# Performance work log

Hardware: AMD Instinct MI355X
Metric: run time of the kernel (lower is better)

Reference implementation:

```python
import jax, jax.numpy as jnp
import numpy as np

BINS = 6
THRESH = 0.2
OUT_HW = (240, 240)


def _normalize(x, lo=0.0, hi=1.0):
    # torch: if max-min==0 return zeros, else affine rescale to [lo, hi]
    mn, mx = x.min(), x.max()
    rng = mx - mn
    safe = jnp.where(rng == 0, 1.0, rng)
    out = (x - mn) / safe * (hi - lo) + lo
    return jnp.where(rng == 0, jnp.zeros_like(x), out)


def _ponder(x):
    w = (x.max() - x.mean()) ** 2
    return _normalize(x) * w


def _zero_border(x):
    # zero first/last row and column (works batched over leading dims)
    return (x.at[..., 0, :].set(0.0)
             .at[..., :, 0].set(0.0)
             .at[..., -1, :].set(0.0)
             .at[..., :, -1].set(0.0))


def _rarity(ch):
    # ch: [H, W] single feature channel
    ch = _zero_border(ch)
    ch = _normalize(ch, 0.0, 256.0)
    # torch.histc(bins=BINS, min=0, max=256): last bin includes the max value
    bin_idx = jnp.clip(jnp.floor(ch / (256.0 / BINS)), 0, BINS - 1).astype(jnp.int32)
    hist = jnp.zeros((BINS,), ch.dtype).at[bin_idx].add(1.0)
    hist = -jnp.log(hist / hist.sum() + 0.0001)
    # (channel * bins - 1).long().clamp(0, bins-1): .long() truncates toward zero
    gidx = jnp.clip(jnp.trunc(ch * BINS - 1.0), 0, BINS - 1).astype(jnp.int32)
    dst = _normalize(hist[gidx], 0.0, 1.0)
    return _ponder(dst)


def _apply_rarity(layer):
    # layer: [1, C, H, W] -> per-channel rarity, ponderated sum, threshold
    ch = layer[0]  # [C, H, W]
    r = jax.vmap(_rarity)(ch)  # [C, H, W]
    rz = _zero_border(r)
    # channel 0 keeps its border (torch code only zeroes borders for i >= 1)
    maps = jnp.concatenate([r[:1], rz[1:]], axis=0)
    proc = jax.vmap(_ponder)(maps).sum(0)
    proc = _normalize(proc, 0.0, 1.0)
    return jnp.where(proc < THRESH, 0.0, proc)


def _group(layer):
    resized = jax.image.resize(_apply_rarity(layer), OUT_HW, 'bilinear')
    # pack of one layer: fuse_itti == map_ponderation of the single map
    return _normalize(_ponder(resized), 0.0, 256.0)


def _forward(l1, l2, l3, l4, l5):
    groups = jnp.stack([_group(l) for l in (l1, l2, l3, l4, l5)], axis=-1)  # [240,240,5]
    return groups.sum(-1), groups


def setup_inputs() -> dict:
    key = jax.random.key(0)
    ks = jax.random.split(key, 5)
    shapes = [(1, 64, 480, 480), (1, 128, 240, 240), (1, 256, 120, 120),
              (1, 512, 60, 60), (1, 512, 30, 30)]
    return {f"l{i+1}": jax.random.uniform(ks[i], shapes[i], jnp.float32)
            for i in range(5)}


def reference(l1, l2, l3, l4, l5):
    return _forward(l1, l2, l3, l4, l5)
```

## Files before the change

kernel.cpp:

```cpp
#include <hip/hip_runtime.h>
#include <math.h>

#define TPB 256

constexpr int DIMS_[5]  = {480, 240, 120, 60, 30};
constexpr int CHS_ [5]  = {64, 128, 256, 512, 512};
constexpr int CHB_ [5]  = {0, 64, 192, 448, 960};
constexpr int TOTCH     = 1472;
constexpr int PROCB_[5] = {0, 230400, 288000, 302400, 306000};
constexpr int PROCTOT   = 306900;

constexpr int O_CHMIN = 0;
constexpr int O_CHMAX = 1472;
constexpr int O_HIST  = 2944;
constexpr int O_GCNT  = 11776;
constexpr int O_CLUT  = 20608;
constexpr int O_BSUM  = O_CLUT + 16 * 1472;
constexpr int O_PMIN  = O_BSUM + 5;
constexpr int O_PMAX  = O_PMIN + 5;
constexpr int O_S3MIN = O_PMAX + 5;
constexpr int O_S3MAX = O_S3MIN + 5;
constexpr int O_S3SUM = O_S3MAX + 5;
constexpr int O_PROC  = 44192;
constexpr int O_RESZ  = O_PROC + PROCTOT;
constexpr int N_INIT  = O_PROC + PROCTOT;

struct P {
  const float* in[5];
  float* ws;
};

__device__ __forceinline__ void mk_hthr(float mn, float rng, float* th) {
  if (rng == 0.0f) { th[0]=th[1]=th[2]=th[3]=th[4]=INFINITY; return; }
  th[0] = mn + rng * (1.0f / 6.0f); th[1] = mn + rng * (2.0f / 6.0f);
  th[2] = mn + rng * (3.0f / 6.0f); th[3] = mn + rng * (4.0f / 6.0f);
  th[4] = mn + rng * (5.0f / 6.0f);
}
__device__ __forceinline__ void mk_gthr(float mn, float rng, float* tg) {
  if (rng == 0.0f) { tg[0]=tg[1]=tg[2]=tg[3]=tg[4]=INFINITY; return; }
  tg[0] = mn + rng * (2.0f / 1536.0f); tg[1] = mn + rng * (3.0f / 1536.0f);
  tg[2] = mn + rng * (4.0f / 1536.0f); tg[3] = mn + rng * (5.0f / 1536.0f);
  tg[4] = mn + rng * (6.0f / 1536.0f);
}

__global__ void k_init(float* ws) {
  int i = blockIdx.x * TPB + threadIdx.x;
  if (i >= N_INIT) return;
  unsigned v = 0u;
  if (i < O_CHMAX) v = 0x7F800000u;
  else if (i >= O_PMIN  && i < O_PMAX)  v = 0x7F800000u;
  else if (i >= O_S3MIN && i < O_S3MAX) v = 0x7F800000u;
  ((unsigned*)ws)[i] = v;
}

template <int L>
__device__ void bodyA(int local, const float* __restrict__ in, float* ws) {
  constexpr int D = DIMS_[L], HW = D * D, HW4 = HW / 4;
  constexpr int BPC = (HW4 + 4095) / 4096;
  int ch = local / BPC, chunk = local % BPC;
  int nvec = HW4 - chunk * 4096; if (nvec > 4096) nvec = 4096;
  const float4* pv = (const float4*)(in + (size_t)ch * HW) + (size_t)chunk * 4096;
  int t = threadIdx.x;
  float mn = INFINITY, mx = 0.0f;
  for (int i = 0; i < 16; i++) {
    int vi = i * TPB + t;
    if (vi < nvec) {
      float4 v = pv[vi];
      float vv[4] = {v.x, v.y, v.z, v.w};
      int e0 = (chunk * 4096 + vi) * 4;
      #pragma unroll
      for (int j = 0; j < 4; j++) {
        int e = e0 + j, y = e / D, x = e - y * D;
        bool inr = ((unsigned)(x - 1) < (unsigned)(D - 2)) && ((unsigned)(y - 1) < (unsigned)(D - 2));
        float s = inr ? vv[j] : 0.0f;
        mn = fminf(mn, s); mx = fmaxf(mx, s);
      }
    }
  }
  for (int o = 32; o; o >>= 1) { mn = fminf(mn, __shfl_down(mn, o)); mx = fmaxf(mx, __shfl_down(mx, o)); }
  __shared__ float smn[4], smx[4];
  int w = t >> 6;
  if ((t & 63) == 0) { smn[w] = mn; smx[w] = mx; }
  __syncthreads();
  if (t == 0) {
    mn = fminf(fminf(smn[0], smn[1]), fminf(smn[2], smn[3]));
    mx = fmaxf(fmaxf(smx[0], smx[1]), fmaxf(smx[2], smx[3]));
    int g = CHB_[L] + ch;
    atomicMin((unsigned*)ws + O_CHMIN + g, __float_as_uint(mn));
    atomicMax((unsigned*)ws + O_CHMAX + g, __float_as_uint(mx));
  }
}
__global__ void kA(P p) {
  int b = blockIdx.x;
  if      (b <  960) bodyA<0>(b,        p.in[0], p.ws);
  else if (b < 1472) bodyA<1>(b -  960, p.in[1], p.ws);
  else if (b < 1728) bodyA<2>(b - 1472, p.in[2], p.ws);
  else if (b < 2240) bodyA<3>(b - 1728, p.in[3], p.ws);
  else               bodyA<4>(b - 2240, p.in[4], p.ws);
}

template <int L>
__device__ void bodyB(int local, const float* __restrict__ in, float* ws) {
  constexpr int D = DIMS_[L], HW = D * D, HW4 = HW / 4;
  constexpr int BPC = (HW4 + 4095) / 4096;
  constexpr int DQ = D / 4;
  int ch = local / BPC, chunk = local % BPC;
  int g = CHB_[L] + ch;
  float mn = ws[O_CHMIN + g], mx = ws[O_CHMAX + g], rng = mx - mn;
  float th[5], tg[5];
  mk_hthr(mn, rng, th);
  mk_gthr(mn, rng, tg);
  int nvec = HW4 - chunk * 4096; if (nvec > 4096) nvec = 4096;
  const float4* pv = (const float4*)(in + (size_t)ch * HW) + (size_t)chunk * 4096;
  int t = threadIdx.x;
  unsigned cH0 = 0, cH1 = 0, cH2 = 0, cH3 = 0, cH4 = 0;
  unsigned cG0 = 0, cG1 = 0, cG2 = 0, cG3 = 0, cG4 = 0, nv4 = 0;
  for (int i = 0; i < 16; i++) {
    int vi = i * TPB + t;
    if (vi < nvec) {
      float4 v = pv[vi];
      float vv[4] = {v.x, v.y, v.z, v.w};
      int f4i = chunk * 4096 + vi;
      if constexpr (D % 4 == 0) {
        int y = f4i / DQ, xq = f4i - y * DQ;
        if (y == 0 || y == D - 1) { vv[0] = vv[1] = vv[2] = vv[3] = 0.0f; }
        else {
          if (xq == 0)      vv[0] = 0.0f;
          if (xq == DQ - 1) vv[3] = 0.0f;
        }
      } else {
        int e0 = f4i * 4;
        #pragma unroll
        for (int j = 0; j < 4; j++) {
          int e = e0 + j, y = e / D, x = e - y * D;
          bool inr = ((unsigned)(x - 1) < (unsigned)(D - 2)) && ((unsigned)(y - 1) < (unsigned)(D - 2));
          if (!inr) vv[j] = 0.0f;
        }
      }
      nv4 += __popcll(__ballot(1));
      #pragma unroll
      for (int j = 0; j < 4; j++) {
        float x = vv[j];
        cH0 += __popcll(__ballot(x >= th[0])); cH1 += __popcll(__ballot(x >= th[1]));
        cH2 += __popcll(__ballot(x >= th[2])); cH3 += __popcll(__ballot(x >= th[3]));
        cH4 += __popcll(__ballot(x >= th[4]));
        cG0 += __popcll(__ballot(x >= tg[0])); cG1 += __popcll(__ballot(x >= tg[1]));
        cG2 += __popcll(__ballot(x >= tg[2])); cG3 += __popcll(__ballot(x >= tg[3]));
        cG4 += __popcll(__ballot(x >= tg[4]));
      }
    }
  }
  if ((t & 63) == 0) {
    unsigned tot = nv4 * 4u;
    unsigned* H = (unsigned*)ws + O_HIST + g * 6;
    unsigned* G = (unsigned*)ws + O_GCNT + g * 6;
    atomicAdd(H + 0, tot - cH0); atomicAdd(H + 1, cH0 - cH1);
    atomicAdd(H + 2, cH1 - cH2); atomicAdd(H + 3, cH2 - cH3);
    atomicAdd(H + 4, cH3 - cH4); atomicAdd(H + 5, cH4);
    atomicAdd(G + 0, tot - cG0); atomicAdd(G + 1, cG0 - cG1);
    atomicAdd(G + 2, cG1 - cG2); atomicAdd(G + 3, cG2 - cG3);
    atomicAdd(G + 4, cG3 - cG4); atomicAdd(G + 5, cG4);
  }
}
__global__ void kB(P p) {
  int b = blockIdx.x;
  if      (b <  960) bodyB<0>(b,        p.in[0], p.ws);
  else if (b < 1472) bodyB<1>(b -  960, p.in[1], p.ws);
  else if (b < 1728) bodyB<2>(b - 1472, p.in[2], p.ws);
  else if (b < 2240) bodyB<3>(b - 1728, p.in[3], p.ws);
  else               bodyB<4>(b - 2240, p.in[4], p.ws);
}

__global__ void kS(P p) {
  int ch = blockIdx.x * TPB + threadIdx.x;
  if (ch >= TOTCH) return;
  float* ws = p.ws;
  int l = (ch < 64) ? 0 : (ch < 192) ? 1 : (ch < 448) ? 2 : (ch < 960) ? 3 : 4;
  int D = DIMS_[l];
  int HW = D * D;
  int c0 = ch - CHB_[l];
  unsigned hc[6], gc[6];
  unsigned* H = (unsigned*)ws + O_HIST + ch * 6;
  unsigned* G = (unsigned*)ws + O_GCNT + ch * 6;
  #pragma unroll
  for (int k = 0; k < 6; k++) { hc[k] = H[k]; gc[k] = G[k]; }
  float HWf = (float)HW;
  float nh[6];
  #pragma unroll
  for (int k = 0; k < 6; k++) nh[k] = -logf((float)hc[k] / HWf + 1e-4f);
  float dmn = INFINITY, dmx = -INFINITY;
  #pragma unroll
  for (int k = 0; k < 6; k++) if (gc[k]) { dmn = fminf(dmn, nh[k]); dmx = fmaxf(dmx, nh[k]); }
  float dr = dmx - dmn;
  float dstn[6];
  #pragma unroll
  for (int k = 0; k < 6; k++) dstn[k] = (dr == 0.0f) ? 0.0f : ((nh[k] - dmn) / dr);
  float maxv = (dr == 0.0f) ? 0.0f : 1.0f;
  double s1 = 0.0;
  #pragma unroll
  for (int k = 0; k < 6; k++) s1 += (double)gc[k] * (double)dstn[k];
  float mean1 = (float)(s1 / (double)HW);
  float w1 = maxv - mean1; w1 *= w1;
  float lut1[6];
  #pragma unroll
  for (int k = 0; k < 6; k++) lut1[k] = dstn[k] * w1;
  float mnc = ws[O_CHMIN + ch], mxc = ws[O_CHMAX + ch];
  float tg[5];
  mk_gthr(mnc, mxc - mnc, tg);
  int gb = (0.0f >= tg[0]) + (0.0f >= tg[1]) + (0.0f >= tg[2]) + (0.0f >= tg[3]) + (0.0f >= tg[4]);
  unsigned bcnt = (unsigned)(4 * D - 4);
  float lmn, lmx;
  double s2 = 0.0;
  if (c0 == 0) {
    lmn = INFINITY; lmx = -INFINITY;
    #pragma unroll
    for (int k = 0; k < 6; k++) if (gc[k]) {
      lmn = fminf(lmn, lut1[k]); lmx = fmaxf(lmx, lut1[k]);
      s2 += (double)gc[k] * (double)lut1[k];
    }
  } else {
    lmn = 0.0f; lmx = 0.0f;
    #pragma unroll
    for (int k = 0; k < 6; k++) {
      unsigned ic = gc[k] - ((k == gb) ? bcnt : 0u);
      if (ic) {
        lmn = fminf(lmn, lut1[k]); lmx = fmaxf(lmx, lut1[k]);
        s2 += (double)ic * (double)lut1[k];
      }
    }
  }
  float mean2 = (float)(s2 / (double)HW);
  float w2 = lmx - mean2; w2 *= w2;
  float r2 = lmx - lmn;
  float lout[6];
  #pragma unroll
  for (int k = 0; k < 6; k++) lout[k] = (r2 == 0.0f) ? 0.0f : (((lut1[k] - lmn) / r2) * w2);
  float* T = ws + O_CLUT + (size_t)ch * 16;
  #pragma unroll
  for (int k = 0; k < 5; k++) T[5 + k] = tg[k];
  #pragma unroll
  for (int k = 0; k < 6; k++) T[10 + k] = lout[k];
  float bc = (c0 == 0) ? lout[gb] : ((r2 == 0.0f) ? 0.0f : (((0.0f - lmn) / r2) * w2));
  atomicAdd(ws + O_BSUM + l, bc);
}

template <int L>
__device__ void bodyC(int local, const float* __restrict__ in, float* ws,
                      float* slut, float* sred) {
  constexpr int D = DIMS_[L], HW = D * D, HW4 = HW / 4, C = CHS_[L];
  constexpr int NT  = (HW4 + 63) / 64;
  constexpr int NCH = C / 64;
  int tile = local % NT, chunk = local / NT;
  int cbase = CHB_[L] + chunk * 64;
  int t = threadIdx.x, lane = t & 63, w = t >> 6;
  const float* gl = ws + O_CLUT + (size_t)cbase * 16;
  for (int i = t; i < 1024; i += TPB) slut[i] = gl[i];
  __syncthreads();
  int p4 = tile * 64 + lane;
  bool valid = p4 < HW4;
  float a0 = 0.0f, a1 = 0.0f, a2 = 0.0f, a3 = 0.0f;
  if (valid) {
    const float4* bp = (const float4*)in + (size_t)(chunk * 64 + w * 16) * HW4 + p4;
    const float* su = slut + (w * 16) * 16;
    #pragma unroll 4
    for (int c = 0; c < 16; c++) {
      float4 v = bp[(size_t)c * HW4];
      const float* cl = su + c * 16 + 5;
      float g0 = cl[0], g1 = cl[1], g2 = cl[2], g3 = cl[3], g4 = cl[4];
      float l0 = cl[5], l1 = cl[6], l2 = cl[7], l3 = cl[8], l4 = cl[9], l5 = cl[10];
      float s;
      s = (v.x >= g0) ? l1 : l0; s = (v.x >= g1) ? l2 : s; s = (v.x >= g2) ? l3 : s;
      s = (v.x >= g3) ? l4 : s;  s = (v.x >= g4) ? l5 : s; a0 += s;
      s = (v.y >= g0) ? l1 : l0; s = (v.y >= g1) ? l2 : s; s = (v.y >= g2) ? l3 : s;
      s = (v.y >= g3) ? l4 : s;  s = (v.y >= g4) ? l5 : s; a1 += s;
      s = (v.z >= g0) ? l1 : l0; s = (v.z >= g1) ? l2 : s; s = (v.z >= g2) ? l3 : s;
      s = (v.z >= g3) ? l4 : s;  s = (v.z >= g4) ? l5 : s; a2 += s;
      s = (v.w >= g0) ? l1 : l0; s = (v.w >= g1) ? l2 : s; s = (v.w >= g2) ? l3 : s;
      s = (v.w >= g3) ? l4 : s;  s = (v.w >= g4) ? l5 : s; a3 += s;
    }
  }
  sred[0 * 256 + w * 64 + lane] = a0;
  sred[1 * 256 + w * 64 + lane] = a1;
  sred[2 * 256 + w * 64 + lane] = a2;
  sred[3 * 256 + w * 64 + lane] = a3;
  __syncthreads();
  if (w == 0 && valid) {
    float o[4];
    #pragma unroll
    for (int j = 0; j < 4; j++)
      o[j] = sred[j * 256 + lane] + sred[j * 256 + 64 + lane] +
             sred[j * 256 + 128 + lane] + sred[j * 256 + 192 + lane];
    float bs = ws[O_BSUM + L];
    float* procL = ws + O_PROC + PROCB_[L];
    int px0 = p4 * 4;
    if constexpr (NCH == 1) {
      #pragma unroll
      for (int j = 0; j < 4; j++) {
        int px = px0 + j, y = px / D, x = px - y * D;
        bool inr = ((unsigned)(x - 1) < (unsigned)(D - 2)) && ((unsigned)(y - 1) < (unsigned)(D - 2));
        if (!inr) o[j] = bs;
      }
      ((float4*)procL)[p4] = make_float4(o[0], o[1], o[2], o[3]);
    } else {
      #pragma unroll
      for (int j = 0; j < 4; j++) {
        int px = px0 + j, y = px / D, x = px - y * D;
        bool inr = ((unsigned)(x - 1) < (unsigned)(D - 2)) && ((unsigned)(y - 1) < (unsigned)(D - 2));
        if (inr) atomicAdd(procL + px, o[j]);
        else if (chunk == 0) procL[px] = bs;
      }
    }
  }
}
__global__ __launch_bounds__(TPB) void kC(P p) {
  __shared__ float slut[1024];
  __shared__ float sred[1024];
  int b = blockIdx.x;
  if      (b <  900) bodyC<0>(b,        p.in[0], p.ws, slut, sred);
  else if (b < 1350) bodyC<1>(b -  900, p.in[1], p.ws, slut, sred);
  else if (b < 1578) bodyC<2>(b - 1350, p.in[2], p.ws, slut, sred);
  else if (b < 1698) bodyC<3>(b - 1578, p.in[3], p.ws, slut, sred);
  else               bodyC<4>(b - 1698, p.in[4], p.ws, slut, sred);
}

template <int L>
__device__ void bodyD(int chunk, float* ws) {
  constexpr int HW = DIMS_[L] * DIMS_[L];
  const float* pr = ws + O_PROC + PROCB_[L];
  int t = threadIdx.x;
  float mn = INFINITY, mx = 0.0f;
  #pragma unroll
  for (int i = 0; i < 16; i++) {
    int idx = chunk * 4096 + i * TPB + t;
    if (idx < HW) { float v = pr[idx]; mn = fminf(mn, v); mx = fmaxf(mx, v); }
  }
  for (int o = 32; o; o >>= 1) { mn = fminf(mn, __shfl_down(mn, o)); mx = fmaxf(mx, __shfl_down(mx, o)); }
  __shared__ float smn[4], smx[4];
  int w = t >> 6;
  if ((t & 63) == 0) { smn[w] = mn; smx[w] = mx; }
  __syncthreads();
  if (t == 0) {
    mn = fminf(fminf(smn[0], smn[1]), fminf(smn[2], smn[3]));
    mx = fmaxf(fmaxf(smx[0], smx[1]), fmaxf(smx[2], smx[3]));
    atomicMin((unsigned*)ws + O_PMIN + L, __float_as_uint(mn));
    atomicMax((unsigned*)ws + O_PMAX + L, __float_as_uint(mx));
  }
}
__global__ void kD(P p) {
  int b = blockIdx.x;
  if      (b < 57) bodyD<0>(b,      p.ws);
  else if (b < 72) bodyD<1>(b - 57, p.ws);
  else if (b < 76) bodyD<2>(b - 72, p.ws);
  else if (b < 77) bodyD<3>(b - 76, p.ws);
  else             bodyD<4>(b - 77, p.ws);
}

template <int L>
__device__ float bodyF(int px, float* ws) {
  constexpr int D = DIMS_[L];
  constexpr float INV = (float)D / 240.0f;
  constexpr float KS = (INV > 1.0f) ? INV : 1.0f;
  int oy = px / 240, ox = px - oy * 240;
  float mnv = __uint_as_float(((unsigned*)ws)[O_PMIN + L]);
  float mxv = __uint_as_float(((unsigned*)ws)[O_PMAX + L]);
  float pr = mxv - mnv;
  const float* procL = ws + O_PROC + PROCB_[L];
  float sfy = ((float)oy + 0.5f) * INV - 0.5f;
  float sfx = ((float)ox + 0.5f) * INV - 0.5f;
  int y0 = (int)ceilf(sfy - KS);  if (y0 < 0) y0 = 0;
  int y1 = (int)floorf(sfy + KS); if (y1 > D - 1) y1 = D - 1;
  int x0 = (int)ceilf(sfx - KS);  if (x0 < 0) x0 = 0;
  int x1 = (int)floorf(sfx + KS); if (x1 > D - 1) x1 = D - 1;
  float wsx = 0.0f;
  for (int jx = x0; jx <= x1; jx++) wsx += fmaxf(1.0f - fabsf(sfx - (float)jx) / KS, 0.0f);
  float acc = 0.0f, wsy = 0.0f;
  for (int jy = y0; jy <= y1; jy++) {
    float wy = fmaxf(1.0f - fabsf(sfy - (float)jy) / KS, 0.0f);
    wsy += wy;
    if (wy > 0.0f) {
      const float* row = procL + jy * D;
      float rs = 0.0f;
      for (int jx = x0; jx <= x1; jx++) {
        float wx = fmaxf(1.0f - fabsf(sfx - (float)jx) / KS, 0.0f);
        if (wx > 0.0f) {
          float v = row[jx];
          float tv = (pr == 0.0f) ? 0.0f : ((v - mnv) / pr);
          tv = (tv < 0.2f) ? 0.0f : tv;
          rs += wx * tv;
        }
      }
      acc += wy * rs;
    }
  }
  return acc / (wsy * wsx);
}
__global__ void kF(P p) {
  float* ws = p.ws;
  int b = blockIdx.x, l = b / 225;
  int px = (b - l * 225) * TPB + threadIdx.x;
  float res;
  switch (l) {
    case 0: res = bodyF<0>(px, ws); break;
    case 1: res = bodyF<1>(px, ws); break;
    case 2: res = bodyF<2>(px, ws); break;
    case 3: res = bodyF<3>(px, ws); break;
    default: res = bodyF<4>(px, ws); break;
  }
  ws[O_RESZ + l * 57600 + px] = res;
  float mn = res, mx = res, s = res;
  for (int o = 32; o; o >>= 1) {
    mn = fminf(mn, __shfl_down(mn, o));
    mx = fmaxf(mx, __shfl_down(mx, o));
    s += __shfl_down(s, o);
  }
  __shared__ float smn[4], smx[4], ssm[4];
  int t = threadIdx.x, w = t >> 6;
  if ((t & 63) == 0) { smn[w] = mn; smx[w] = mx; ssm[w] = s; }
  __syncthreads();
  if (t == 0) {
    mn = fminf(fminf(smn[0], smn[1]), fminf(smn[2], smn[3]));
    mx = fmaxf(fmaxf(smx[0], smx[1]), fmaxf(smx[2], smx[3]));
    s = ssm[0] + ssm[1] + ssm[2] + ssm[3];
    atomicMin((unsigned*)ws + O_S3MIN + l, __float_as_uint(mn));
    atomicMax((unsigned*)ws + O_S3MAX + l, __float_as_uint(mx));
    atomicAdd(ws + O_S3SUM + l, s);
  }
}

__global__ void kG2(P p, float* __restrict__ out) {
  float* ws = p.ws;
  int px = blockIdx.x * TPB + threadIdx.x;
  float sum = 0.0f;
  #pragma unroll
  for (int l = 0; l < 5; l++) {
    float v = ws[O_RESZ + l * 57600 + px];
    float mn3 = __uint_as_float(((unsigned*)ws)[O_S3MIN + l]);
    float mx3 = __uint_as_float(((unsigned*)ws)[O_S3MAX + l]);
    float mean3 = ws[O_S3SUM + l] / 57600.0f;
    float r3 = mx3 - mn3;
    float ov;
    if (r3 == 0.0f) ov = 0.0f;
    else {
      float w3 = mx3 - mean3; w3 *= w3;
      if (w3 == 0.0f) ov = 0.0f;
      else ov = ((v - mn3) / r3) * w3 / w3 * 256.0f;
    }
    out[57600 + px * 5 + l] = ov;
    sum += ov;
  }
  out[px] = sum;
}

extern "C" void kernel_launch(void* const* d_in, const int* in_sizes, int n_in,
                              void* d_out, int out_size, void* d_ws, size_t ws_size,
                              hipStream_t stream) {
  (void)in_sizes; (void)n_in; (void)out_size; (void)ws_size;
  P p;
  for (int i = 0; i < 5; i++) p.in[i] = (const float*)d_in[i];
  p.ws = (float*)d_ws;
  float* out = (float*)d_out;

  k_init<<<(N_INIT + TPB - 1) / TPB, TPB, 0, stream>>>(p.ws);
  kA  <<<2752, TPB, 0, stream>>>(p);
  kB  <<<2752, TPB, 0, stream>>>(p);
  kS  <<<6,    TPB, 0, stream>>>(p);
  kC  <<<1730, TPB, 0, stream>>>(p);
  kD  <<<78,   TPB, 0, stream>>>(p);
  kF  <<<1125, TPB, 0, stream>>>(p);
  kG2 <<<225,  TPB, 0, stream>>>(p, out);
}
```

Measured before the change: 294.0 us.

## Batch loads in stats passes, fuse layer-0 proc min/max into kC, shrink init

The min/max and histogram passes now issue four float4 loads up front before reducing, which raises memory-level parallelism. Border zeroing moves into a shared helper. For layer 0 (a single chunk per pixel), kC computes the proc min/max with wave shuffles and atomics as it writes, so kD no longer reads back the large 480x480 map. k_init now zeroes only the proc region that multi-chunk layers accumulate into. Out-of-range lanes in kB are filled with -inf so the ballot counts stay correct.

New measurement: 314.0 us. 6.8% more time.

```diff
diff --git a/kernel.cpp b/kernel.cpp
--- a/kernel.cpp
+++ b/kernel.cpp
@@ -23,7 +23,9 @@
 constexpr int O_S3SUM = O_S3MAX + 5;
 constexpr int O_PROC  = 44192;
 constexpr int O_RESZ  = O_PROC + PROCTOT;
-constexpr int N_INIT  = O_PROC + PROCTOT;
+constexpr int N_STAT  = O_PROC;
+constexpr int N_PZ    = PROCTOT - PROCB_[1];
+constexpr int N_INIT  = N_STAT + N_PZ;
 
 struct P {
   const float* in[5];
@@ -43,14 +45,40 @@
   tg[4] = mn + rng * (6.0f / 1536.0f);
 }
 
+template <int D>
+__device__ __forceinline__ void border_zero_f4(int f4i, float4& v) {
+  constexpr int DQ = D / 4;
+  if constexpr (D % 4 == 0) {
+    int y = f4i / DQ, xq = f4i - y * DQ;
+    if (y == 0 || y == D - 1) { v.x = v.y = v.z = v.w = 0.0f; }
+    else {
+      if (xq == 0)      v.x = 0.0f;
+      if (xq == DQ - 1) v.w = 0.0f;
+    }
+  } else {
+    int e0 = f4i * 4;
+    float* c = (float*)&v;
+    #pragma unroll
+    for (int j = 0; j < 4; j++) {
+      int e = e0 + j, y = e / D, x = e - y * D;
+      bool inr = ((unsigned)(x - 1) < (unsigned)(D - 2)) && ((unsigned)(y - 1) < (unsigned)(D - 2));
+      if (!inr) c[j] = 0.0f;
+    }
+  }
+}
+
 __global__ void k_init(float* ws) {
   int i = blockIdx.x * TPB + threadIdx.x;
   if (i >= N_INIT) return;
-  unsigned v = 0u;
-  if (i < O_CHMAX) v = 0x7F800000u;
-  else if (i >= O_PMIN  && i < O_PMAX)  v = 0x7F800000u;
-  else if (i >= O_S3MIN && i < O_S3MAX) v = 0x7F800000u;
-  ((unsigned*)ws)[i] = v;
+  if (i < N_STAT) {
+    unsigned v = 0u;
+    if (i < O_CHMAX) v = 0x7F800000u;
+    else if (i >= O_PMIN  && i < O_PMAX)  v = 0x7F800000u;
+    else if (i >= O_S3MIN && i < O_S3MAX) v = 0x7F800000u;
+    ((unsigned*)ws)[i] = v;
+  } else {
+    ws[O_PROC + PROCB_[1] + (i - N_STAT)] = 0.0f;
+  }
 }
 
 template <int L>
@@ -58,23 +86,27 @@
   constexpr int D = DIMS_[L], HW = D * D, HW4 = HW / 4;
   constexpr int BPC = (HW4 + 4095) / 4096;
   int ch = local / BPC, chunk = local % BPC;
-  int nvec = HW4 - chunk * 4096; if (nvec > 4096) nvec = 4096;
-  const float4* pv = (const float4*)(in + (size_t)ch * HW) + (size_t)chunk * 4096;
+  int base = chunk * 4096;
+  int nvec = HW4 - base; if (nvec > 4096) nvec = 4096;
+  const float4* pv = (const float4*)(in + (size_t)ch * HW) + base;
   int t = threadIdx.x;
   float mn = INFINITY, mx = 0.0f;
-  for (int i = 0; i < 16; i++) {
-    int vi = i * TPB + t;
-    if (vi < nvec) {
-      float4 v = pv[vi];
-      float vv[4] = {v.x, v.y, v.z, v.w};
-      int e0 = (chunk * 4096 + vi) * 4;
-      #pragma unroll
-      for (int j = 0; j < 4; j++) {
-        int e = e0 + j, y = e / D, x = e - y * D;
-        bool inr = ((unsigned)(x - 1) < (unsigned)(D - 2)) && ((unsigned)(y - 1) < (unsigned)(D - 2));
-        float s = inr ? vv[j] : 0.0f;
-        mn = fminf(mn, s); mx = fmaxf(mx, s);
-      }
+  for (int o = 0; o < 4; o++) {
+    float4 v[4];
+    #pragma unroll
+    for (int q = 0; q < 4; q++) {
+      int vi = (o * 4 + q) * TPB + t;
+      float4 vv = make_float4(0.0f, 0.0f, 0.0f, 0.0f);
+      if (vi < nvec) {
+        vv = pv[vi];
+        border_zero_f4<D>(base + vi, vv);
+      }
+      v[q] = vv;
+    }
+    #pragma unroll
+    for (int q = 0; q < 4; q++) {
+      mn = fminf(mn, fminf(fminf(v[q].x, v[q].y), fminf(v[q].z, v[q].w)));
+      mx = fmaxf(mx, fmaxf(fmaxf(v[q].x, v[q].y), fmaxf(v[q].z, v[q].w)));
     }
   }
   for (int o = 32; o; o >>= 1) { mn = fminf(mn, __shfl_down(mn, o)); mx = fmaxf(mx, __shfl_down(mx, o)); }
@@ -103,41 +135,35 @@
 __device__ void bodyB(int local, const float* __restrict__ in, float* ws) {
   constexpr int D = DIMS_[L], HW = D * D, HW4 = HW / 4;
   constexpr int BPC = (HW4 + 4095) / 4096;
-  constexpr int DQ = D / 4;
   int ch = local / BPC, chunk = local % BPC;
   int g = CHB_[L] + ch;
   float mn = ws[O_CHMIN + g], mx = ws[O_CHMAX + g], rng = mx - mn;
   float th[5], tg[5];
   mk_hthr(mn, rng, th);
   mk_gthr(mn, rng, tg);
-  int nvec = HW4 - chunk * 4096; if (nvec > 4096) nvec = 4096;
-  const float4* pv = (const float4*)(in + (size_t)ch * HW) + (size_t)chunk * 4096;
+  int base = chunk * 4096;
+  int nvec = HW4 - base; if (nvec > 4096) nvec = 4096;
+  const float4* pv = (const float4*)(in + (size_t)ch * HW) + base;
   int t = threadIdx.x;
   unsigned cH0 = 0, cH1 = 0, cH2 = 0, cH3 = 0, cH4 = 0;
   unsigned cG0 = 0, cG1 = 0, cG2 = 0, cG3 = 0, cG4 = 0, nv4 = 0;
-  for (int i = 0; i < 16; i++) {
-    int vi = i * TPB + t;
-    if (vi < nvec) {
-      float4 v = pv[vi];
-      float vv[4] = {v.x, v.y, v.z, v.w};
-      int f4i = chunk * 4096 + vi;
-      if constexpr (D % 4 == 0) {
-        int y = f4i / DQ, xq = f4i - y * DQ;
-        if (y == 0 || y == D - 1) { vv[0] = vv[1] = vv[2] = vv[3] = 0.0f; }
-        else {
-          if (xq == 0)      vv[0] = 0.0f;
-          if (xq == DQ - 1) vv[3] = 0.0f;
-        }
-      } else {
-        int e0 = f4i * 4;
-        #pragma unroll
-        for (int j = 0; j < 4; j++) {
-          int e = e0 + j, y = e / D, x = e - y * D;
-          bool inr = ((unsigned)(x - 1) < (unsigned)(D - 2)) && ((unsigned)(y - 1) < (unsigned)(D - 2));
-          if (!inr) vv[j] = 0.0f;
-        }
-      }
-      nv4 += __popcll(__ballot(1));
+  for (int o = 0; o < 4; o++) {
+    float4 v[4];
+    #pragma unroll
+    for (int q = 0; q < 4; q++) {
+      int vi = (o * 4 + q) * TPB + t;
+      float4 vv = make_float4(-INFINITY, -INFINITY, -INFINITY, -INFINITY);
+      if (vi < nvec) {
+        vv = pv[vi];
+        border_zero_f4<D>(base + vi, vv);
+      }
+      v[q] = vv;
+    }
+    #pragma unroll
+    for (int q = 0; q < 4; q++) {
+      int vi = (o * 4 + q) * TPB + t;
+      nv4 += __popcll(__ballot(vi < nvec));
+      float vv[4] = {v[q].x, v[q].y, v[q].z, v[q].w};
       #pragma unroll
       for (int j = 0; j < 4; j++) {
         float x = vv[j];
@@ -284,7 +310,7 @@
   sred[2 * 256 + w * 64 + lane] = a2;
   sred[3 * 256 + w * 64 + lane] = a3;
   __syncthreads();
-  if (w == 0 && valid) {
+  if (w == 0) {
     float o[4];
     #pragma unroll
     for (int j = 0; j < 4; j++)
@@ -294,14 +320,24 @@
     float* procL = ws + O_PROC + PROCB_[L];
     int px0 = p4 * 4;
     if constexpr (NCH == 1) {
-      #pragma unroll
-      for (int j = 0; j < 4; j++) {
-        int px = px0 + j, y = px / D, x = px - y * D;
-        bool inr = ((unsigned)(x - 1) < (unsigned)(D - 2)) && ((unsigned)(y - 1) < (unsigned)(D - 2));
-        if (!inr) o[j] = bs;
-      }
-      ((float4*)procL)[p4] = make_float4(o[0], o[1], o[2], o[3]);
-    } else {
+      float mn = INFINITY, mx = 0.0f;
+      if (valid) {
+        #pragma unroll
+        for (int j = 0; j < 4; j++) {
+          int px = px0 + j, y = px / D, x = px - y * D;
+          bool inr = ((unsigned)(x - 1) < (unsigned)(D - 2)) && ((unsigned)(y - 1) < (unsigned)(D - 2));
+          if (!inr) o[j] = bs;
+        }
+        ((float4*)procL)[p4] = make_float4(o[0], o[1], o[2], o[3]);
+        mn = fminf(fminf(o[0], o[1]), fminf(o[2], o[3]));
+        mx = fmaxf(fmaxf(o[0], o[1]), fmaxf(o[2], o[3]));
+      }
+      for (int s = 32; s; s >>= 1) { mn = fminf(mn, __shfl_down(mn, s)); mx = fmaxf(mx, __shfl_down(mx, s)); }
+      if (lane == 0) {
+        atomicMin((unsigned*)ws + O_PMIN + L, __float_as_uint(mn));
+        atomicMax((unsigned*)ws + O_PMAX + L, __float_as_uint(mx));
+      }
+    } else if (valid) {
       #pragma unroll
       for (int j = 0; j < 4; j++) {
         int px = px0 + j, y = px / D, x = px - y * D;
@@ -348,11 +384,10 @@
 }
 __global__ void kD(P p) {
   int b = blockIdx.x;
-  if      (b < 57) bodyD<0>(b,      p.ws);
-  else if (b < 72) bodyD<1>(b - 57, p.ws);
-  else if (b < 76) bodyD<2>(b - 72, p.ws);
-  else if (b < 77) bodyD<3>(b - 76, p.ws);
-  else             bodyD<4>(b - 77, p.ws);
+  if      (b < 15) bodyD<1>(b,      p.ws);
+  else if (b < 19) bodyD<2>(b - 15, p.ws);
+  else if (b < 20) bodyD<3>(b - 19, p.ws);
+  else             bodyD<4>(b - 20, p.ws);
 }
 
 template <int L>
@@ -465,7 +500,7 @@
   kB  <<<2752, TPB, 0, stream>>>(p);
   kS  <<<6,    TPB, 0, stream>>>(p);
   kC  <<<1730, TPB, 0, stream>>>(p);
-  kD  <<<78,   TPB, 0, stream>>>(p);
+  kD  <<<21,   TPB, 0, stream>>>(p);
   kF  <<<1125, TPB, 0, stream>>>(p);
   kG2 <<<225,  TPB, 0, stream>>>(p, out);
 }
```
